# Kernel tuning notes

Measured on AMD Instinct MI355X. Metric: run time of the kernel, lower is better.

Reference implementation:

```python
import jax, jax.numpy as jnp
import numpy as np

BN_EPS = 1e-3  # keras BatchNormalization default epsilon


def batch_norm(x):
    # Fresh keras BatchNorm in training mode: gamma=1, beta=0, batch stats over axis 0
    mean = jnp.mean(x, axis=0, keepdims=True)
    var = jnp.var(x, axis=0, keepdims=True)
    return (x - mean) * jax.lax.rsqrt(var + BN_EPS)


def setup_inputs() -> dict:
    key = jax.random.key(0)
    k1, k2, k3 = jax.random.split(key, 3)
    N, D = 100000, 512
    x1 = jax.random.normal(k1, (N, D), dtype=jnp.float32)
    x2 = jax.random.normal(k2, (N, D), dtype=jnp.float32)
    # glorot_uniform for [D, D] kernel
    limit = np.sqrt(6.0 / (D + D)).astype(np.float32)
    kernel = jax.random.uniform(k3, (D, D), dtype=jnp.float32, minval=-limit, maxval=limit)
    return {"x1": x1, "x2": x2, "kernel": kernel}


def reference(x1, x2, kernel):
    b1 = batch_norm(x1)  # [N, D]
    b2 = batch_norm(x2)  # [N, D]
    gate = jax.nn.relu(jnp.tanh(b1 @ kernel))  # [N, D]; dropout_rate=0 -> no dropout
    out = jnp.tanh(b2 * (1.0 - gate) + b1 * gate)
    return out
```

## Files before the change

### kernel.cpp

```cpp
#include <hip/hip_runtime.h>
#include <hip/hip_fp16.h>
#include <stdint.h>

#define N_ROWS 100000
#define DCOLS 512
#define BN_EPS 1e-3f
#define PB 256

typedef __attribute__((ext_vector_type(8))) _Float16 f16x8;
typedef __attribute__((ext_vector_type(4))) float f32x4;
typedef __attribute__((ext_vector_type(4))) unsigned short u16x4;
typedef __attribute__((ext_vector_type(4))) unsigned int u32x4;

__device__ inline float fast_tanh(float x) {
  float e = __expf(2.0f * x);
  return 1.0f - 2.0f * __builtin_amdgcn_rcpf(e + 1.0f);
}
__device__ inline void gld16(const void* g, void* l) {
  __builtin_amdgcn_global_load_lds(
      (const __attribute__((address_space(1))) void*)g,
      (__attribute__((address_space(3))) void*)l, 16, 0, 0);
}
__device__ inline unsigned int h2u(__half2 h) {
  unsigned int u;
  __builtin_memcpy(&u, &h, 4);
  return u;
}
__device__ inline f16x8 u2f(const u32x4& u) {
  f16x8 h;
  __builtin_memcpy(&h, &u, 16);
  return h;
}

__device__ inline void split8h(const float4& v0, const float4& v1,
                               f16x8& hi8, f16x8& lo8) {
  __half2 h0 = __floats2half2_rn(v0.x, v0.y);
  __half2 h1 = __floats2half2_rn(v0.z, v0.w);
  __half2 h2 = __floats2half2_rn(v1.x, v1.y);
  __half2 h3 = __floats2half2_rn(v1.z, v1.w);
  __half2 l0 = __floats2half2_rn(v0.x - __low2float(h0), v0.y - __high2float(h0));
  __half2 l1 = __floats2half2_rn(v0.z - __low2float(h1), v0.w - __high2float(h1));
  __half2 l2 = __floats2half2_rn(v1.x - __low2float(h2), v1.y - __high2float(h2));
  __half2 l3 = __floats2half2_rn(v1.z - __low2float(h3), v1.w - __high2float(h3));
  u32x4 hi = (u32x4){h2u(h0), h2u(h1), h2u(h2), h2u(h3)};
  u32x4 lo = (u32x4){h2u(l0), h2u(l1), h2u(l2), h2u(l3)};
  hi8 = u2f(hi);
  lo8 = u2f(lo);
}

__global__ __launch_bounds__(256) void k_stats_partial(
    const float* __restrict__ x1, const float* __restrict__ x2,
    float* __restrict__ psum, float* __restrict__ psq) {
  const int CH = (N_ROWS + PB - 1) / PB;
  int bx = blockIdx.x;
  int arr = blockIdx.y;
  const float* x = arr ? x2 : x1;
  int r0 = bx * CH;
  int r1 = min(N_ROWS, r0 + CH);
  int c0 = threadIdx.x * 2;
  float s0 = 0.f, s1 = 0.f, q0 = 0.f, q1 = 0.f;
#pragma unroll 8
  for (int r = r0; r < r1; ++r) {
    float2 v = *(const float2*)(x + (size_t)r * DCOLS + c0);
    s0 += v.x; s1 += v.y;
    q0 += v.x * v.x; q1 += v.y * v.y;
  }
  size_t base = ((size_t)(arr * PB + bx)) * DCOLS + c0;
  psum[base] = s0; psum[base + 1] = s1;
  psq[base]  = q0; psq[base + 1]  = q1;
}

__global__ __launch_bounds__(512) void k_stats_final(
    const float* __restrict__ psum, const float* __restrict__ psq,
    float* __restrict__ stats) {
  int a = blockIdx.x;
  int c = threadIdx.x;
  float sa[8], qa[8];
#pragma unroll
  for (int u = 0; u < 8; ++u) { sa[u] = 0.f; qa[u] = 0.f; }
  for (int b = 0; b < PB; b += 8) {
#pragma unroll
    for (int u = 0; u < 8; ++u) {
      size_t base = ((size_t)(a * PB + b + u)) * DCOLS + c;
      sa[u] += psum[base];
      qa[u] += psq[base];
    }
  }
  float s = ((sa[0]+sa[1])+(sa[2]+sa[3]))+((sa[4]+sa[5])+(sa[6]+sa[7]));
  float q = ((qa[0]+qa[1])+(qa[2]+qa[3]))+((qa[4]+qa[5])+(qa[6]+qa[7]));
  float inv = 1.0f / (float)N_ROWS;
  float mean = s * inv;
  float var = q * inv - mean * mean;
  float scale = rsqrtf(var + BN_EPS);
  stats[a * 1024 + c] = scale;
  stats[a * 1024 + 512 + c] = -mean * scale;
}

__global__ __launch_bounds__(256) void k_prepw(
    const float* __restrict__ wk, const float* __restrict__ stats,
    u32x4* __restrict__ wf) {
  int gid = blockIdx.x * 256 + threadIdx.x;
  int j = gid & 511;
  int kg = gid >> 9;
  int k0 = kg * 8;
  unsigned short h[8];
#pragma unroll
  for (int u = 0; u < 8; ++u) {
    float w = wk[(size_t)(k0 + u) * DCOLS + j] * stats[k0 + u];
    __half hh = __float2half_rn(w);
    h[u] = __half_as_ushort(hh);
  }
  int slice = k0 >> 5;
  int lr = (k0 >> 3) & 3;
  int lane = (lr << 4) | (j & 15);
  int g = j >> 4;
  int idx = slice * 2048 + g * 64 + lane;
  u16x4* ph = (u16x4*)&wf[idx];
  u16x4 h0 = {h[0], h[1], h[2], h[3]};
  u16x4 h1 = {h[4], h[5], h[6], h[7]};
  ph[0] = h0; ph[1] = h1;
}

__global__ __launch_bounds__(512) void k_c_partial(
    const float* __restrict__ wk, const float* __restrict__ stats,
    float* __restrict__ cpart) {
  int b = blockIdx.x;
  int j = threadIdx.x;
  const float* negms1 = stats + 512;
  float acc = 0.f;
#pragma unroll
  for (int u = 0; u < 8; ++u) {
    int k = b * 8 + u;
    acc += negms1[k] * wk[(size_t)k * DCOLS + j];
  }
  cpart[b * DCOLS + j] = acc;
}

__global__ __launch_bounds__(512) void k_c_final(
    const float* __restrict__ cpart, float* __restrict__ cvec) {
  int j = threadIdx.x;
  float a = 0.f;
  for (int b = 0; b < 64; ++b) a += cpart[b * DCOLS + j];
  cvec[j] = a;
}

__global__ __launch_bounds__(512, 4) void k_main(
    const float* __restrict__ x1, const float* __restrict__ x2,
    const float* __restrict__ stats, const float* __restrict__ cvec,
    const u32x4* __restrict__ wf, float* __restrict__ out) {
  __shared__ char smem[65536];

  const int tid = threadIdx.x;
  const int lane = tid & 63;
  const int wv = tid >> 6;
  const int ra = lane & 15;
  const int rq = lane >> 4;

  const int xcd = blockIdx.x & 7;
  const int wgid = xcd * 782 + (blockIdx.x >> 3);
  const int panel = wgid >> 3;
  const int oc = wgid & 7;
  const int row0 = panel * 128;
  const int col0 = oc * 64;

  int arow = row0 + wv * 16 + ra;
  arow = min(arow, N_ROWS - 1);
  const float* abase = x1 + (size_t)arow * DCOLS + rq * 8;

#pragma unroll
  for (int u = 0; u < 8; ++u) {
    int id = u * 8 + wv;
    int slice = id >> 2, cg = id & 3;
    const u32x4* src =
        wf + (size_t)slice * 2048 + (size_t)(oc * 4 + cg) * 64 + lane;
    gld16(src, smem + id * 1024);
  }

  f32x4 acc[4];
#pragma unroll
  for (int cg = 0; cg < 4; ++cg) {
    float cj = cvec[col0 + cg * 16 + ra];
    acc[cg] = (f32x4){cj, cj, cj, cj};
  }

  float4 av[2][4];

  auto loadA = [&](int s, int pset) {
    const float* p = abase + s * 64;
    av[pset][0] = *(const float4*)(p);
    av[pset][1] = *(const float4*)(p + 4);
    av[pset][2] = *(const float4*)(p + 32);
    av[pset][3] = *(const float4*)(p + 36);
  };

  loadA(0, 0);
  asm volatile("s_waitcnt vmcnt(0)" ::: "memory");
  __builtin_amdgcn_s_barrier();
  __builtin_amdgcn_sched_barrier(0);

#pragma unroll
  for (int s = 0; s < 8; ++s) {
    const int p = s & 1;
    if (s < 7) loadA(s + 1, p ^ 1);
#pragma unroll
    for (int kk = 0; kk < 2; ++kk) {
      f16x8 bfr[4];
#pragma unroll
      for (int cg = 0; cg < 4; ++cg)
        bfr[cg] = *(const f16x8*)(smem + ((s * 2 + kk) * 4 + cg) * 1024 +
                                  lane * 16);
      f16x8 ah, al;
      split8h(av[p][kk * 2], av[p][kk * 2 + 1], ah, al);
      __builtin_amdgcn_s_setprio(1);
#pragma unroll
      for (int cg = 0; cg < 4; ++cg)
        acc[cg] = __builtin_amdgcn_mfma_f32_16x16x32_f16(ah, bfr[cg], acc[cg],
                                                         0, 0, 0);
#pragma unroll
      for (int cg = 0; cg < 4; ++cg)
        acc[cg] = __builtin_amdgcn_mfma_f32_16x16x32_f16(al, bfr[cg], acc[cg],
                                                         0, 0, 0);
      __builtin_amdgcn_s_setprio(0);
    }
  }

  const float* scale1 = stats;
  const float* negms1 = stats + 512;
  const float* scale2 = stats + 1024;
  const float* negms2 = stats + 1536;

  float s1j[4], n1j[4], s2j[4], n2j[4];
#pragma unroll
  for (int cg = 0; cg < 4; ++cg) {
    int j = col0 + cg * 16 + ra;
    s1j[cg] = scale1[j]; n1j[cg] = negms1[j];
    s2j[cg] = scale2[j]; n2j[cg] = negms2[j];
  }
#pragma unroll
  for (int r = 0; r < 4; ++r) {
    int n = row0 + wv * 16 + rq * 4 + r;
    if (n < N_ROWS) {
#pragma unroll
      for (int cg = 0; cg < 4; ++cg) {
        int j = col0 + cg * 16 + ra;
        float c = acc[cg][r];
        float tt = fast_tanh(c);
        float gt = fmaxf(tt, 0.0f);
        size_t idx = (size_t)n * DCOLS + j;
        float b1v = fmaf(x1[idx], s1j[cg], n1j[cg]);
        float b2v = fmaf(x2[idx], s2j[cg], n2j[cg]);
        out[idx] = fast_tanh(b2v + gt * (b1v - b2v));
      }
    }
  }
}

extern "C" void kernel_launch(void* const* d_in, const int* in_sizes, int n_in,
                              void* d_out, int out_size, void* d_ws, size_t ws_size,
                              hipStream_t stream) {
  const float* x1 = (const float*)d_in[0];
  const float* x2 = (const float*)d_in[1];
  const float* wk = (const float*)d_in[2];
  float* out = (float*)d_out;
  char* ws = (char*)d_ws;

  if (ws_size < (size_t)(4u << 20)) return;

  float* psum  = (float*)ws;
  float* psq   = (float*)(ws + (1 << 20));
  float* stats = (float*)(ws + (2 << 20));
  float* cpart = (float*)(ws + (2 << 20) + (16 << 10));
  float* cvec  = (float*)(ws + (2 << 20) + (160 << 10));
  u32x4* wf    = (u32x4*)(ws + (3 << 20));

  k_stats_partial<<<dim3(PB, 2), 256, 0, stream>>>(x1, x2, psum, psq);
  k_stats_final<<<2, 512, 0, stream>>>(psum, psq, stats);
  k_prepw<<<128, 256, 0, stream>>>(wk, stats, wf);
  k_c_partial<<<64, 512, 0, stream>>>(wk, stats, cpart);
  k_c_final<<<1, 512, 0, stream>>>(cpart, cvec);

  const int nblocks = 8 * 782;
  k_main<<<nblocks, 512, 0, stream>>>(x1, x2, stats, cvec, wf, out);
}
```

Measured before the change: 360.4 us.

## Widen main-kernel tile to 128 columns with double-buffered streamed weight slices

Each workgroup now covers a 128x128 output tile instead of 128x64, with 8 waves arranged 4x2 so that every wave computes a 32x64 subtile. Each A fragment is reused across more columns, and the grid shrinks by half. The full 64KB weight preload is replaced by a 16KB double-buffered LDS ring, streaming one K-slice per step with barriers between steps, which lowers LDS use and may raise occupancy. In exchange, the kernel adds per-step barriers and more accumulator registers.

```diff
diff --git a/kernel.cpp b/kernel.cpp
--- a/kernel.cpp
+++ b/kernel.cpp
@@ -148,79 +148,103 @@
     const float* __restrict__ x1, const float* __restrict__ x2,
     const float* __restrict__ stats, const float* __restrict__ cvec,
     const u32x4* __restrict__ wf, float* __restrict__ out) {
-  __shared__ char smem[65536];
+  __shared__ char smem[16384];
 
   const int tid = threadIdx.x;
   const int lane = tid & 63;
   const int wv = tid >> 6;
+  const int wr = wv >> 1;
+  const int wc = wv & 1;
   const int ra = lane & 15;
   const int rq = lane >> 4;
 
   const int xcd = blockIdx.x & 7;
-  const int wgid = xcd * 782 + (blockIdx.x >> 3);
-  const int panel = wgid >> 3;
-  const int oc = wgid & 7;
+  const int wgid = xcd * 391 + (blockIdx.x >> 3);
+  const int panel = wgid >> 2;
+  const int q = wgid & 3;
   const int row0 = panel * 128;
-  const int col0 = oc * 64;
-
-  int arow = row0 + wv * 16 + ra;
-  arow = min(arow, N_ROWS - 1);
-  const float* abase = x1 + (size_t)arow * DCOLS + rq * 8;
-
-#pragma unroll
-  for (int u = 0; u < 8; ++u) {
-    int id = u * 8 + wv;
-    int slice = id >> 2, cg = id & 3;
-    const u32x4* src =
-        wf + (size_t)slice * 2048 + (size_t)(oc * 4 + cg) * 64 + lane;
-    gld16(src, smem + id * 1024);
-  }
-
-  f32x4 acc[4];
+  const int col0 = q * 128;
+
+  const float* abase[2];
+#pragma unroll
+  for (int rg = 0; rg < 2; ++rg) {
+    int r = row0 + wr * 32 + rg * 16 + ra;
+    r = min(r, N_ROWS - 1);
+    abase[rg] = x1 + (size_t)r * DCOLS + rq * 8;
+  }
+
+  const u32x4* bsrc = wf + (size_t)(q * 8 + wv) * 64 + lane;
+  const int bdst = wv * 1024;
+
+  f32x4 acc[2][4];
 #pragma unroll
   for (int cg = 0; cg < 4; ++cg) {
-    float cj = cvec[col0 + cg * 16 + ra];
-    acc[cg] = (f32x4){cj, cj, cj, cj};
+    float cj = cvec[col0 + wc * 64 + cg * 16 + ra];
+#pragma unroll
+    for (int rg = 0; rg < 2; ++rg) acc[rg][cg] = (f32x4){cj, cj, cj, cj};
   }
 
   float4 av[2][4];
 
+  auto stageB = [&](int s, int buf) {
+    gld16(bsrc + (size_t)s * 2048, smem + buf * 8192 + bdst);
+  };
   auto loadA = [&](int s, int pset) {
-    const float* p = abase + s * 64;
-    av[pset][0] = *(const float4*)(p);
-    av[pset][1] = *(const float4*)(p + 4);
-    av[pset][2] = *(const float4*)(p + 32);
-    av[pset][3] = *(const float4*)(p + 36);
+#pragma unroll
+    for (int rg = 0; rg < 2; ++rg) {
+      const float* p = abase[rg] + s * 32;
+      av[pset][rg * 2 + 0] = *(const float4*)(p);
+      av[pset][rg * 2 + 1] = *(const float4*)(p + 4);
+    }
   };
 
+  stageB(0, 0);
+  asm volatile("" ::: "memory");
   loadA(0, 0);
-  asm volatile("s_waitcnt vmcnt(0)" ::: "memory");
+  asm volatile("s_waitcnt vmcnt(4)" ::: "memory");
   __builtin_amdgcn_s_barrier();
   __builtin_amdgcn_sched_barrier(0);
 
 #pragma unroll
-  for (int s = 0; s < 8; ++s) {
+  for (int s = 0; s < 16; ++s) {
     const int p = s & 1;
-    if (s < 7) loadA(s + 1, p ^ 1);
-#pragma unroll
-    for (int kk = 0; kk < 2; ++kk) {
-      f16x8 bfr[4];
-#pragma unroll
-      for (int cg = 0; cg < 4; ++cg)
-        bfr[cg] = *(const f16x8*)(smem + ((s * 2 + kk) * 4 + cg) * 1024 +
-                                  lane * 16);
-      f16x8 ah, al;
-      split8h(av[p][kk * 2], av[p][kk * 2 + 1], ah, al);
-      __builtin_amdgcn_s_setprio(1);
-#pragma unroll
-      for (int cg = 0; cg < 4; ++cg)
-        acc[cg] = __builtin_amdgcn_mfma_f32_16x16x32_f16(ah, bfr[cg], acc[cg],
-                                                         0, 0, 0);
-#pragma unroll
-      for (int cg = 0; cg < 4; ++cg)
-        acc[cg] = __builtin_amdgcn_mfma_f32_16x16x32_f16(al, bfr[cg], acc[cg],
-                                                         0, 0, 0);
-      __builtin_amdgcn_s_setprio(0);
+    if (s < 15) {
+      stageB(s + 1, p ^ 1);
+      asm volatile("" ::: "memory");
+      loadA(s + 1, p ^ 1);
+      __builtin_amdgcn_sched_barrier(0);
+    }
+    f16x8 bfr[4];
+#pragma unroll
+    for (int cg = 0; cg < 4; ++cg)
+      bfr[cg] = *(const f16x8*)(smem + p * 8192 + (wc * 4 + cg) * 1024 +
+                                lane * 16);
+    f16x8 ah0, al0, ah1, al1;
+    split8h(av[p][0], av[p][1], ah0, al0);
+    split8h(av[p][2], av[p][3], ah1, al1);
+    __builtin_amdgcn_s_setprio(1);
+#pragma unroll
+    for (int cg = 0; cg < 4; ++cg)
+      acc[0][cg] = __builtin_amdgcn_mfma_f32_16x16x32_f16(ah0, bfr[cg],
+                                                          acc[0][cg], 0, 0, 0);
+#pragma unroll
+    for (int cg = 0; cg < 4; ++cg)
+      acc[1][cg] = __builtin_amdgcn_mfma_f32_16x16x32_f16(ah1, bfr[cg],
+                                                          acc[1][cg], 0, 0, 0);
+#pragma unroll
+    for (int cg = 0; cg < 4; ++cg)
+      acc[0][cg] = __builtin_amdgcn_mfma_f32_16x16x32_f16(al0, bfr[cg],
+                                                          acc[0][cg], 0, 0, 0);
+#pragma unroll
+    for (int cg = 0; cg < 4; ++cg)
+      acc[1][cg] = __builtin_amdgcn_mfma_f32_16x16x32_f16(al1, bfr[cg],
+                                                          acc[1][cg], 0, 0, 0);
+    __builtin_amdgcn_s_setprio(0);
+
+    if (s < 15) {
+      asm volatile("s_waitcnt vmcnt(4) lgkmcnt(0)" ::: "memory");
+      __builtin_amdgcn_s_barrier();
+      __builtin_amdgcn_sched_barrier(0);
     }
   }
 
@@ -232,24 +256,27 @@
   float s1j[4], n1j[4], s2j[4], n2j[4];
 #pragma unroll
   for (int cg = 0; cg < 4; ++cg) {
-    int j = col0 + cg * 16 + ra;
+    int j = col0 + wc * 64 + cg * 16 + ra;
     s1j[cg] = scale1[j]; n1j[cg] = negms1[j];
     s2j[cg] = scale2[j]; n2j[cg] = negms2[j];
   }
 #pragma unroll
-  for (int r = 0; r < 4; ++r) {
-    int n = row0 + wv * 16 + rq * 4 + r;
-    if (n < N_ROWS) {
-#pragma unroll
-      for (int cg = 0; cg < 4; ++cg) {
-        int j = col0 + cg * 16 + ra;
-        float c = acc[cg][r];
-        float tt = fast_tanh(c);
-        float gt = fmaxf(tt, 0.0f);
-        size_t idx = (size_t)n * DCOLS + j;
-        float b1v = fmaf(x1[idx], s1j[cg], n1j[cg]);
-        float b2v = fmaf(x2[idx], s2j[cg], n2j[cg]);
-        out[idx] = fast_tanh(b2v + gt * (b1v - b2v));
+  for (int rg = 0; rg < 2; ++rg) {
+#pragma unroll
+    for (int r = 0; r < 4; ++r) {
+      int n = row0 + wr * 32 + rg * 16 + rq * 4 + r;
+      if (n < N_ROWS) {
+#pragma unroll
+        for (int cg = 0; cg < 4; ++cg) {
+          int j = col0 + wc * 64 + cg * 16 + ra;
+          float c = acc[rg][cg][r];
+          float tt = fast_tanh(c);
+          float gt = fmaxf(tt, 0.0f);
+          size_t idx = (size_t)n * DCOLS + j;
+          float b1v = fmaf(x1[idx], s1j[cg], n1j[cg]);
+          float b2v = fmaf(x2[idx], s2j[cg], n2j[cg]);
+          out[idx] = fast_tanh(b2v + gt * (b1v - b2v));
+        }
       }
     }
   }
@@ -279,6 +306,6 @@
   k_c_partial<<<64, 512, 0, stream>>>(wk, stats, cpart);
   k_c_final<<<1, 512, 0, stream>>>(cpart, cvec);
 
-  const int nblocks = 8 * 782;
+  const int nblocks = 8 * 391;
   k_main<<<nblocks, 512, 0, stream>>>(x1, x2, stats, cvec, wf, out);
 }
```

Result: slower. 387.6 us (+7.5%).
